# Kernel tuning notes

Hardware: AMD Instinct MI355X
Metric: run time of the kernel (lower is better)

The kernel has to match this reference:

```python
import jax, jax.numpy as jnp
import numpy as np
import math

NUM_BUCKETS = 32
MAX_DISTANCE = 128
N_HEADS = 16
D_KV = 64


def _relative_position_bucket(relative_position, num_buckets=NUM_BUCKETS, max_distance=MAX_DISTANCE):
    # bidirectional (encoder) variant
    num_buckets //= 2
    relative_buckets = (relative_position > 0).astype(jnp.int32) * num_buckets
    rp = jnp.abs(relative_position)
    max_exact = num_buckets // 2
    is_small = rp < max_exact
    rp_large = max_exact + (
        jnp.log(jnp.maximum(rp, 1).astype(jnp.float32) / max_exact)
        / math.log(max_distance / max_exact)
        * (num_buckets - max_exact)
    ).astype(jnp.int32)
    rp_large = jnp.minimum(rp_large, num_buckets - 1)
    return relative_buckets + jnp.where(is_small, rp, rp_large)


def compute_bias(rel_bias, q_len, k_len):
    ctx = jnp.arange(q_len)[:, None]
    mem = jnp.arange(k_len)[None, :]
    buckets = _relative_position_bucket(mem - ctx)          # [q, k]
    values = rel_bias[buckets]                               # [q, k, h]
    return jnp.transpose(values, (2, 0, 1))[None]            # [1, h, q, k]


def setup_inputs() -> dict:
    key = jax.random.key(0)
    ks = jax.random.split(key, 6)
    d_model, inner = 1024, N_HEADS * D_KV
    s = 0.02
    return {
        "hidden_states": jax.random.normal(ks[0], (2, 2048, d_model), jnp.float32),
        "Wq": jax.random.normal(ks[1], (d_model, inner), jnp.float32) * s,
        "Wk": jax.random.normal(ks[2], (d_model, inner), jnp.float32) * s,
        "Wv": jax.random.normal(ks[3], (d_model, inner), jnp.float32) * s,
        "Wo": jax.random.normal(ks[4], (inner, d_model), jnp.float32) * s,
        "rel_bias": jax.random.normal(ks[5], (NUM_BUCKETS, N_HEADS), jnp.float32) * s,
    }


def reference(hidden_states, Wq, Wk, Wv, Wo, rel_bias):
    B, S, D = hidden_states.shape

    def split_heads(x):  # [B,S,inner] -> [B,H,S,dk]
        return x.reshape(B, S, N_HEADS, D_KV).transpose(0, 2, 1, 3)

    q = split_heads(hidden_states @ Wq)
    k = split_heads(hidden_states @ Wk)
    v = split_heads(hidden_states @ Wv)

    # T5 does NOT scale by 1/sqrt(d_kv)
    scores = jnp.einsum("bhqd,bhkd->bhqk", q, k)
    scores = scores + compute_bias(rel_bias, S, S)
    attn = jax.nn.softmax(scores, axis=-1)
    ctx = jnp.einsum("bhqk,bhkd->bhqd", attn, v)
    ctx = ctx.transpose(0, 2, 1, 3).reshape(B, S, N_HEADS * D_KV)
    return ctx @ Wo
```

## Files before the change

### kernel.cpp

```cpp
#include <hip/hip_runtime.h>
#include <hip/hip_bf16.h>

typedef __bf16 bf16x8 __attribute__((ext_vector_type(8)));
typedef __bf16 bf16x4 __attribute__((ext_vector_type(4)));
typedef float floatx4 __attribute__((ext_vector_type(4)));
typedef float floatx16 __attribute__((ext_vector_type(16)));
using bf16 = __hip_bfloat16;

#define S_    2048
#define NHEAD 16
#define LOG2E 1.4426950408889634f

__device__ __forceinline__ void load_lds16(const bf16* g, void* lds) {
  __builtin_amdgcn_global_load_lds((const __attribute__((address_space(1))) void*)g,
                                   (__attribute__((address_space(3))) void*)lds, 16, 0, 0);
}

__global__ void prep_kernel(const float* __restrict__ hidden,
                            const float* __restrict__ wq, const float* __restrict__ wk,
                            const float* __restrict__ wv, const float* __restrict__ wo,
                            const float* __restrict__ rel_bias,
                            bf16* __restrict__ hbf, bf16* __restrict__ wt_qkv,
                            bf16* __restrict__ wt_o, float* __restrict__ tab) {
  __shared__ bf16 tile[32][33];
  int bid = blockIdx.x;
  if (bid < 4096) {
    int i = (bid * 256 + threadIdx.x) * 4;
    float4 v = *(const float4*)(hidden + i);
    bf16 o[4] = {__float2bfloat16(v.x), __float2bfloat16(v.y),
                 __float2bfloat16(v.z), __float2bfloat16(v.w)};
    *(uint2*)(hbf + i) = *(const uint2*)o;
  } else if (bid < 8192) {
    int r = bid - 4096;
    int mat = r >> 10;
    int rem = r & 1023;
    int n0 = (rem & 31) * 32, k0 = (rem >> 5) * 32;
    int tx = threadIdx.x & 31, ty = threadIdx.x >> 5;
    const float* src = (mat == 0) ? wq : (mat == 1) ? wk : (mat == 2) ? wv : wo;
    bf16* dst = (mat == 3) ? wt_o : wt_qkv + mat * 1024 * 1024;
#pragma unroll
    for (int j = 0; j < 32; j += 8)
      tile[ty + j][tx] = __float2bfloat16(src[(k0 + ty + j) * 1024 + n0 + tx]);
    __syncthreads();
#pragma unroll
    for (int j = 0; j < 32; j += 8)
      dst[(n0 + ty + j) * 1024 + k0 + tx] = tile[tx][ty + j];
  } else {
    int idx = (bid - 8192) * 256 + threadIdx.x;
    int h = idx >> 12, j = idx & 4095;
    int delta = j - 2048;
    int rb = (delta > 0) ? 16 : 0;
    int rpa = delta < 0 ? -delta : delta;
    int bsmall;
    if (rpa < 8) {
      bsmall = rpa;
    } else {
      int lg = 25 - __clz(rpa * rpa);
      bsmall = 8 + lg;
      if (bsmall > 15) bsmall = 15;
    }
    tab[idx] = rel_bias[(rb + bsmall) * 16 + h] * LOG2E;
  }
}

__global__ __launch_bounds__(256) void gemm_qkv_kernel(const bf16* __restrict__ A,
                                                       const bf16* __restrict__ Bt,
                                                       bf16* __restrict__ qh,
                                                       bf16* __restrict__ kf,
                                                       bf16* __restrict__ vf) {
  const int K = 1024;
  __shared__ bf16 As[128 * 32];
  __shared__ bf16 Bs[128 * 32];
  int t = threadIdx.x;
  int m0 = blockIdx.y * 128, n0 = blockIdx.x * 128;
  int w = t >> 6, lane = t & 63, ln = lane & 15, quad = lane >> 4;
  int wr = w >> 1, wc = w & 1;
  floatx4 acc[4][4];
  floatx4 zero = {0.f, 0.f, 0.f, 0.f};
#pragma unroll
  for (int i = 0; i < 4; i++)
#pragma unroll
    for (int j = 0; j < 4; j++) acc[i][j] = zero;

  int r = t >> 2, c = (t & 3) * 8;
  const bf16* Ag = A + (long)(m0 + r) * K + c;
  const bf16* Bg = Bt + (long)(n0 + r) * K + c;
  char* ldsA0 = (char*)As + w * 1024;
  char* ldsA1 = ldsA0 + 4096;
  char* ldsB0 = (char*)Bs + w * 1024;
  char* ldsB1 = ldsB0 + 4096;

  for (int k0 = 0; k0 < K; k0 += 32) {
    load_lds16(Ag + k0, ldsA0);
    load_lds16(Ag + (long)64 * K + k0, ldsA1);
    load_lds16(Bg + k0, ldsB0);
    load_lds16(Bg + (long)64 * K + k0, ldsB1);
    __syncthreads();
    bf16x8 af[4], bfv[4];
#pragma unroll
    for (int i = 0; i < 4; i++)
      af[i] = *(const bf16x8*)&As[(wr * 64 + i * 16 + ln) * 32 + quad * 8];
#pragma unroll
    for (int j = 0; j < 4; j++)
      bfv[j] = *(const bf16x8*)&Bs[(wc * 64 + j * 16 + ln) * 32 + quad * 8];
#pragma unroll
    for (int i = 0; i < 4; i++)
#pragma unroll
      for (int j = 0; j < 4; j++)
        acc[i][j] = __builtin_amdgcn_mfma_f32_16x16x32_bf16(af[i], bfv[j], acc[i][j], 0, 0, 0);
    __syncthreads();
  }

  int nb = n0 + wc * 64;
  int type = nb >> 10, h = (nb >> 6) & 15;
  int b = (m0 >> 11);
  int sl0 = (m0 & 2047) + wr * 64;
  long bhbase = (long)((b * 16 + h)) * 131072;

  if (type == 0) {
#pragma unroll
    for (int i = 0; i < 4; i++)
#pragma unroll
      for (int j = 0; j < 4; j++) {
        int d = j * 16 + ln;
#pragma unroll
        for (int rr = 0; rr < 4; rr++) {
          int s = sl0 + i * 16 + quad * 4 + rr;
          qh[bhbase + (long)s * 64 + d] = __float2bfloat16(acc[i][j][rr]);
        }
      }
  } else if (type == 1) {
#pragma unroll
    for (int i = 0; i < 4; i++)
#pragma unroll
      for (int j = 0; j < 4; j++) {
        long base = bhbase + sl0 * 64 + (i >> 1) * 2048 + j * 512 + (ln >> 3) * 256 +
                    (i & 1) * 128 + quad * 32 + (ln & 7);
#pragma unroll
        for (int rr = 0; rr < 4; rr++)
          kf[base + rr * 8] = __float2bfloat16(acc[i][j][rr]);
      }
  } else {
#pragma unroll
    for (int i = 0; i < 4; i++)
#pragma unroll
      for (int j = 0; j < 4; j++) {
        long off = sl0 * 64 + i * 1024 + (j >> 1) * 512 + (quad >> 1) * 256 +
                   ((j & 1) * 16 + ln) * 8 + (quad & 1) * 4;
        bf16x4 pk = {(__bf16)acc[i][j][0], (__bf16)acc[i][j][1],
                     (__bf16)acc[i][j][2], (__bf16)acc[i][j][3]};
        *(bf16x4*)(vf + bhbase + off) = pk;
      }
  }
}

#define LOADKV(Kr, Vr, kk)                                        \
  {                                                               \
    const bf16* kp = kfb + (kk) * 64 + loff;                      \
    const bf16* vp = vfb + (kk) * 64 + loff;                      \
    Kr[0] = *(const bf16x8*)(kp);                                 \
    Kr[1] = *(const bf16x8*)(kp + 512);                           \
    Kr[2] = *(const bf16x8*)(kp + 1024);                          \
    Kr[3] = *(const bf16x8*)(kp + 1536);                          \
    Vr[0] = *(const bf16x8*)(vp);                                 \
    Vr[1] = *(const bf16x8*)(vp + 512);                           \
    Vr[2] = *(const bf16x8*)(vp + 1024);                          \
    Vr[3] = *(const bf16x8*)(vp + 1536);                          \
  }

#define COMPUTE(Kr, Vr, kk)                                                       \
  {                                                                               \
    floatx16 st = zf;                                                             \
    __builtin_amdgcn_s_setprio(1);                                                \
    st = __builtin_amdgcn_mfma_f32_32x32x16_bf16(Kr[0], Qf[0], st, 0, 0, 0);      \
    st = __builtin_amdgcn_mfma_f32_32x32x16_bf16(Kr[1], Qf[1], st, 0, 0, 0);      \
    st = __builtin_amdgcn_mfma_f32_32x32x16_bf16(Kr[2], Qf[2], st, 0, 0, 0);      \
    st = __builtin_amdgcn_mfma_f32_32x32x16_bf16(Kr[3], Qf[3], st, 0, 0, 0);      \
    __builtin_amdgcn_s_setprio(0);                                                \
    float p[16];                                                                  \
    bool near = ((kk) > qw - 160) && ((kk) < qw + 160);                           \
    if (near) {                                                                   \
      int kb = (kk) + 4 * h5 - (qw + l31) + 2048;                                 \
      _Pragma("unroll")                                                           \
      for (int r = 0; r < 16; r++)                                                \
        p[r] = __builtin_amdgcn_exp2f(                                            \
            fmaf(st[r], LOG2E, bt[kb + (r & 3) + 8 * (r >> 2)]));                 \
    } else {                                                                      \
      float cb = ((kk) > qw) ? cpos : cneg;                                       \
      _Pragma("unroll")                                                           \
      for (int r = 0; r < 16; r++)                                                \
        p[r] = __builtin_amdgcn_exp2f(fmaf(st[r], LOG2E, cb));                    \
    }                                                                             \
    float a0 = (p[0] + p[1]) + (p[2] + p[3]);                                     \
    float a1 = (p[4] + p[5]) + (p[6] + p[7]);                                     \
    float a2 = (p[8] + p[9]) + (p[10] + p[11]);                                   \
    float a3 = (p[12] + p[13]) + (p[14] + p[15]);                                 \
    l_acc += (a0 + a1) + (a2 + a3);                                               \
    unsigned d[8];                                                                \
    _Pragma("unroll")                                                             \
    for (int i = 0; i < 8; i++)                                                   \
      asm("v_cvt_pk_bf16_f32 %0, %1, %2" : "=v"(d[i]) : "v"(p[2*i]), "v"(p[2*i+1])); \
    unsigned w0 = d[0], w2 = d[2];                                                \
    asm("v_permlane32_swap_b32 %0, %1" : "+v"(w0), "+v"(w2));                     \
    unsigned w1 = d[1], w3 = d[3];                                                \
    asm("v_permlane32_swap_b32 %0, %1" : "+v"(w1), "+v"(w3));                     \
    unsigned w4 = d[4], w6 = d[6];                                                \
    asm("v_permlane32_swap_b32 %0, %1" : "+v"(w4), "+v"(w6));                     \
    unsigned w5 = d[5], w7 = d[7];                                                \
    asm("v_permlane32_swap_b32 %0, %1" : "+v"(w5), "+v"(w7));                     \
    union { unsigned u[4]; bf16x8 v; } a0u, a1u;                                  \
    a0u.u[0] = w0; a0u.u[1] = w1; a0u.u[2] = w2; a0u.u[3] = w3;                   \
    a1u.u[0] = w4; a1u.u[1] = w5; a1u.u[2] = w6; a1u.u[3] = w7;                   \
    __builtin_amdgcn_s_setprio(1);                                                \
    o0 = __builtin_amdgcn_mfma_f32_32x32x16_bf16(a0u.v, Vr[0], o0, 0, 0, 0);      \
    o1 = __builtin_amdgcn_mfma_f32_32x32x16_bf16(a0u.v, Vr[1], o1, 0, 0, 0);      \
    o0 = __builtin_amdgcn_mfma_f32_32x32x16_bf16(a1u.v, Vr[2], o0, 0, 0, 0);      \
    o1 = __builtin_amdgcn_mfma_f32_32x32x16_bf16(a1u.v, Vr[3], o1, 0, 0, 0);      \
    __builtin_amdgcn_s_setprio(0);                                                \
  }

__global__ __launch_bounds__(256, 2) void attn_kernel(const bf16* __restrict__ qh,
                                                      const bf16* __restrict__ kf,
                                                      const bf16* __restrict__ vf,
                                                      const float* __restrict__ btab,
                                                      bf16* __restrict__ ctx) {
  int t = threadIdx.x, w = t >> 6, lane = t & 63;
  int l31 = lane & 31, h5 = lane >> 5;
  int bh = blockIdx.y, b = bh >> 4, h = bh & 15;
  int qw = blockIdx.x * 128 + w * 32;

  const bf16* qbase = qh + (long)bh * S_ * 64;
  const bf16* kfb = kf + (long)bh * S_ * 64;
  const bf16* vfb = vf + (long)bh * S_ * 64;
  const float* bt = btab + h * 4096;
  int loff = h5 * 256 + l31 * 8;

  bf16x8 Qf[4];
#pragma unroll
  for (int ds = 0; ds < 4; ds++)
    Qf[ds] = *(const bf16x8*)(qbase + (long)(qw + l31) * 64 + ds * 16 + h5 * 8);

  float cneg = bt[0], cpos = bt[4095];
  float l_acc = 0.f;
  floatx16 zf = {0.f, 0.f, 0.f, 0.f, 0.f, 0.f, 0.f, 0.f,
                 0.f, 0.f, 0.f, 0.f, 0.f, 0.f, 0.f, 0.f};
  floatx16 o0 = zf, o1 = zf;

  bf16x8 Ka[4], Va[4], Kb[4], Vb[4];
  LOADKV(Ka, Va, 0);
  LOADKV(Kb, Vb, 32);

  for (int k0 = 0; k0 < S_; k0 += 64) {
    COMPUTE(Ka, Va, k0);
    if (k0 + 64 < S_) LOADKV(Ka, Va, k0 + 64);
    COMPUTE(Kb, Vb, k0 + 32);
    if (k0 + 96 < S_) LOADKV(Kb, Vb, k0 + 96);
  }

  l_acc += __shfl_xor(l_acc, 32);
  float linv = 1.0f / l_acc;
#pragma unroll
  for (int r = 0; r < 16; r++) {
    int qrow = (r & 3) + 8 * (r >> 2) + 4 * h5;
    float lv = __shfl(linv, qrow);
    int q = qw + qrow;
    long base = (long)(b * S_ + q) * 1024 + h * 64 + l31;
    ctx[base] = __float2bfloat16(o0[r] * lv);
    ctx[base + 32] = __float2bfloat16(o1[r] * lv);
  }
}

__global__ __launch_bounds__(256) void gemm_bt_kernel(const bf16* __restrict__ A,
                                                      const bf16* __restrict__ Bt,
                                                      float* __restrict__ C,
                                                      int M, int N, int K) {
  __shared__ bf16 As[128 * 32];
  __shared__ bf16 Bs[128 * 32];
  int t = threadIdx.x;
  int m0 = blockIdx.y * 128, n0 = blockIdx.x * 128;
  int w = t >> 6, lane = t & 63, ln = lane & 15, quad = lane >> 4;
  int wr = w >> 1, wc = w & 1;
  floatx4 acc[4][4];
  floatx4 zero = {0.f, 0.f, 0.f, 0.f};
#pragma unroll
  for (int i = 0; i < 4; i++)
#pragma unroll
    for (int j = 0; j < 4; j++) acc[i][j] = zero;

  int r = t >> 2, c = (t & 3) * 8;
  const bf16* Ag = A + (long)(m0 + r) * K + c;
  const bf16* Bg = Bt + (long)(n0 + r) * K + c;
  char* ldsA0 = (char*)As + w * 1024;
  char* ldsA1 = ldsA0 + 4096;
  char* ldsB0 = (char*)Bs + w * 1024;
  char* ldsB1 = ldsB0 + 4096;

  for (int k0 = 0; k0 < K; k0 += 32) {
    load_lds16(Ag + k0, ldsA0);
    load_lds16(Ag + (long)64 * K + k0, ldsA1);
    load_lds16(Bg + k0, ldsB0);
    load_lds16(Bg + (long)64 * K + k0, ldsB1);
    __syncthreads();
    bf16x8 af[4], bfv[4];
#pragma unroll
    for (int i = 0; i < 4; i++)
      af[i] = *(const bf16x8*)&As[(wr * 64 + i * 16 + ln) * 32 + quad * 8];
#pragma unroll
    for (int j = 0; j < 4; j++)
      bfv[j] = *(const bf16x8*)&Bs[(wc * 64 + j * 16 + ln) * 32 + quad * 8];
#pragma unroll
    for (int i = 0; i < 4; i++)
#pragma unroll
      for (int j = 0; j < 4; j++)
        acc[i][j] = __builtin_amdgcn_mfma_f32_16x16x32_bf16(af[i], bfv[j], acc[i][j], 0, 0, 0);
    __syncthreads();
  }

#pragma unroll
  for (int i = 0; i < 4; i++)
#pragma unroll
    for (int j = 0; j < 4; j++)
#pragma unroll
      for (int rr = 0; rr < 4; rr++)
        C[(long)(m0 + wr * 64 + i * 16 + quad * 4 + rr) * N + n0 + wc * 64 + j * 16 + ln] =
            acc[i][j][rr];
}

extern "C" void kernel_launch(void* const* d_in, const int* in_sizes, int n_in,
                              void* d_out, int out_size, void* d_ws, size_t ws_size,
                              hipStream_t stream) {
  (void)in_sizes; (void)n_in; (void)out_size; (void)ws_size;
  const float* hidden   = (const float*)d_in[0];
  const float* Wq       = (const float*)d_in[1];
  const float* Wk       = (const float*)d_in[2];
  const float* Wv       = (const float*)d_in[3];
  const float* Wo       = (const float*)d_in[4];
  const float* rel_bias = (const float*)d_in[5];

  char* ws = (char*)d_ws;
  bf16*  hbf    = (bf16*)(ws + 0);
  bf16*  wt_qkv = (bf16*)(ws + 8388608);
  bf16*  wt_o   = (bf16*)(ws + 14680064);
  float* btab   = (float*)(ws + 16777216);
  bf16*  qh     = (bf16*)(ws + 17039360);
  bf16*  kf     = (bf16*)(ws + 25427968);
  bf16*  vf     = (bf16*)(ws + 33816576);
  bf16*  ctx    = (bf16*)(ws + 42205184);

  prep_kernel<<<dim3(8448), dim3(256), 0, stream>>>(hidden, Wq, Wk, Wv, Wo, rel_bias,
                                                    hbf, wt_qkv, wt_o, btab);
  gemm_qkv_kernel<<<dim3(24, 32), dim3(256), 0, stream>>>(hbf, wt_qkv, qh, kf, vf);
  attn_kernel<<<dim3(16, 32), dim3(256), 0, stream>>>(qh, kf, vf, btab, ctx);
  gemm_bt_kernel<<<dim3(8, 32), dim3(256), 0, stream>>>(ctx, wt_o, (float*)d_out, 4096, 1024, 1024);
}
```

Baseline: 195.2 us.

## Split attention key range across waves and map blocks to XCDs

Each attention block now covers 64 queries with four waves. Two waves take the first half of the keys and two take the second half, and the partial outputs and row sums are combined through LDS before normalisation. The grid becomes a flat 1024 blocks whose index is remapped so that blocks sharing a batch-head land on the same XCD. Launch bounds are raised to allow four blocks per CU. The aim is more parallelism and better L2 reuse of K/V, at the cost of an LDS reduction, a barrier, and register pressure under the tighter launch bound.

```diff
diff --git a/kernel.cpp b/kernel.cpp
--- a/kernel.cpp
+++ b/kernel.cpp
@@ -219,15 +219,22 @@
     __builtin_amdgcn_s_setprio(0);                                                \
   }
 
-__global__ __launch_bounds__(256, 2) void attn_kernel(const bf16* __restrict__ qh,
+__global__ __launch_bounds__(256, 4) void attn_kernel(const bf16* __restrict__ qh,
                                                       const bf16* __restrict__ kf,
                                                       const bf16* __restrict__ vf,
                                                       const float* __restrict__ btab,
                                                       bf16* __restrict__ ctx) {
+  __shared__ float mbuf[2][64][33];
   int t = threadIdx.x, w = t >> 6, lane = t & 63;
   int l31 = lane & 31, h5 = lane >> 5;
-  int bh = blockIdx.y, b = bh >> 4, h = bh & 15;
-  int qw = blockIdx.x * 128 + w * 32;
+
+  int lin = blockIdx.x;
+  int xcd = lin & 7, j = lin >> 3;
+  int bh = xcd * 4 + (j >> 5);
+  int qblk = j & 31;
+  int b = bh >> 4, h = bh & 15;
+  int qw = qblk * 64 + (w & 1) * 32;
+  int kbeg = (w >> 1) * 1024;
 
   const bf16* qbase = qh + (long)bh * S_ * 64;
   const bf16* kfb = kf + (long)bh * S_ * 64;
@@ -247,26 +254,41 @@
   floatx16 o0 = zf, o1 = zf;
 
   bf16x8 Ka[4], Va[4], Kb[4], Vb[4];
-  LOADKV(Ka, Va, 0);
-  LOADKV(Kb, Vb, 32);
-
-  for (int k0 = 0; k0 < S_; k0 += 64) {
+  LOADKV(Ka, Va, kbeg);
+  LOADKV(Kb, Vb, kbeg + 32);
+
+  int kend = kbeg + 1024;
+  for (int k0 = kbeg; k0 < kend; k0 += 64) {
     COMPUTE(Ka, Va, k0);
-    if (k0 + 64 < S_) LOADKV(Ka, Va, k0 + 64);
+    if (k0 + 64 < kend) LOADKV(Ka, Va, k0 + 64);
     COMPUTE(Kb, Vb, k0 + 32);
-    if (k0 + 96 < S_) LOADKV(Kb, Vb, k0 + 96);
+    if (k0 + 96 < kend) LOADKV(Kb, Vb, k0 + 96);
   }
 
   l_acc += __shfl_xor(l_acc, 32);
-  float linv = 1.0f / l_acc;
-#pragma unroll
-  for (int r = 0; r < 16; r++) {
-    int qrow = (r & 3) + 8 * (r >> 2) + 4 * h5;
-    float lv = __shfl(linv, qrow);
-    int q = qw + qrow;
-    long base = (long)(b * S_ + q) * 1024 + h * 64 + l31;
-    ctx[base] = __float2bfloat16(o0[r] * lv);
-    ctx[base + 32] = __float2bfloat16(o1[r] * lv);
+
+  if (w >= 2) {
+    float* dst = &mbuf[w & 1][lane][0];
+#pragma unroll
+    for (int r = 0; r < 16; r++) { dst[r] = o0[r]; dst[16 + r] = o1[r]; }
+    dst[32] = l_acc;
+  }
+  __syncthreads();
+  if (w < 2) {
+    const float* src = &mbuf[w][lane][0];
+#pragma unroll
+    for (int r = 0; r < 16; r++) { o0[r] += src[r]; o1[r] += src[16 + r]; }
+    l_acc += src[32];
+    float linv = 1.0f / l_acc;
+#pragma unroll
+    for (int r = 0; r < 16; r++) {
+      int qrow = (r & 3) + 8 * (r >> 2) + 4 * h5;
+      float lv = __shfl(linv, qrow);
+      int q = qw + qrow;
+      long base = (long)(b * S_ + q) * 1024 + h * 64 + l31;
+      ctx[base] = __float2bfloat16(o0[r] * lv);
+      ctx[base + 32] = __float2bfloat16(o1[r] * lv);
+    }
   }
 }
 
@@ -350,6 +372,6 @@
   prep_kernel<<<dim3(8448), dim3(256), 0, stream>>>(hidden, Wq, Wk, Wv, Wo, rel_bias,
                                                     hbf, wt_qkv, wt_o, btab);
   gemm_qkv_kernel<<<dim3(24, 32), dim3(256), 0, stream>>>(hbf, wt_qkv, qh, kf, vf);
-  attn_kernel<<<dim3(16, 32), dim3(256), 0, stream>>>(qh, kf, vf, btab, ctx);
+  attn_kernel<<<dim3(1024), dim3(256), 0, stream>>>(qh, kf, vf, btab, ctx);
   gemm_bt_kernel<<<dim3(8, 32), dim3(256), 0, stream>>>(ctx, wt_o, (float*)d_out, 4096, 1024, 1024);
 }
```

After: 403.0 us. 2.06x slower.
